# Kernel tuning notes

Hardware: AMD Instinct MI355X
Metric: run time of the kernel (lower is better)

Reference implementation:

```python
import jax, jax.numpy as jnp
import numpy as np

N = 100000          # num nodes
E = 3200000         # num edges (avg degree 32)
C = 64              # num_classes
L = 10000           # num labeled nodes
NUM_LAYERS = 10
ALPHA = 0.9


def setup_inputs() -> dict:
    key = jax.random.key(0)
    k1, k2, k3, k4 = jax.random.split(key, 4)
    y_soft = jax.random.normal(k1, (N, C), dtype=jnp.float32)
    y_true = jax.random.randint(k2, (L,), 0, C)
    mask = jax.random.randint(k3, (L,), 0, N)
    edge_index = jax.random.randint(k4, (2, E), 0, N)
    return {"y_soft": y_soft, "y_true": y_true, "mask": mask,
            "edge_index": edge_index}


def reference(y_soft, y_true, mask, edge_index):
    row, col = edge_index[0], edge_index[1]  # source -> target

    # smooth(): normalize predictions, then clamp labeled nodes to one-hot y
    z = jax.nn.softmax(y_soft, axis=1)                       # [N, C]
    y_onehot = jax.nn.one_hot(y_true, C, dtype=z.dtype)      # [L, C]
    z = z.at[mask].set(y_onehot)

    # gcn_norm without self-loops: w_e = deg^-1/2[row] * deg^-1/2[col]
    ones = jnp.ones((edge_index.shape[1],), dtype=z.dtype)
    deg = jax.ops.segment_sum(ones, col, num_segments=N)     # [N]
    dinv = jnp.where(deg > 0,
                     jax.lax.rsqrt(jnp.maximum(deg, 1e-12)),
                     jnp.zeros_like(deg))
    norm = dinv[row] * dinv[col]                             # [E]

    # Label spreading: Z <- clip(alpha * (D^-1/2 A D^-1/2) Z + (1-alpha) Z0, 0, 1)
    res = (1.0 - ALPHA) * z
    out = z
    for _ in range(NUM_LAYERS):
        msg = norm[:, None] * out[row]                       # [E, C] gather
        agg = jax.ops.segment_sum(msg, col, num_segments=N)  # [N, C] scatter-add
        out = jnp.clip(ALPHA * agg + res, 0.0, 1.0)          # PyG post_step clamp
    return out
```

## Files before the change

kernel.cpp:

```cpp
#include <hip/hip_runtime.h>
#include <hip/hip_fp16.h>

#define NCLS 64
#define ALPHA 0.9f
#define SCAN_BS 256
#define SCAN_CHUNK 1024
#define NBUCK 256
#define BSHIFT 9
#define BSPAN 512
#define P1_CAP 3200

__device__ __forceinline__ float wave_max64(float v) {
    #pragma unroll
    for (int o = 32; o > 0; o >>= 1) v = fmaxf(v, __shfl_xor(v, o, 64));
    return v;
}
__device__ __forceinline__ float wave_sum64(float v) {
    #pragma unroll
    for (int o = 32; o > 0; o >>= 1) v += __shfl_xor(v, o, 64);
    return v;
}

__global__ void winner_k(const int* __restrict__ mask, int* __restrict__ winner, int L) {
    int i = blockIdx.x * blockDim.x + threadIdx.x;
    if (i < L) atomicMax(&winner[mask[i]], i);
}

__global__ void deg_k(const int* __restrict__ col, int* __restrict__ deg, int E) {
    int stride = gridDim.x * blockDim.x;
    for (int e = blockIdx.x * blockDim.x + threadIdx.x; e < E; e += stride)
        atomicAdd(&deg[col[e]], 1);
}

__global__ void dinv_k(const int* __restrict__ deg, float* __restrict__ dinv, int n_nodes) {
    int i = blockIdx.x * blockDim.x + threadIdx.x;
    if (i < n_nodes) {
        int d = deg[i];
        dinv[i] = (d > 0) ? rsqrtf((float)d) : 0.0f;
    }
}

__global__ void scan_local_k(const int* __restrict__ deg, int* __restrict__ rowptr,
                             int* __restrict__ bsum, int n) {
    __shared__ int lds[SCAN_BS];
    int base = blockIdx.x * SCAN_CHUNK;
    int t = threadIdx.x;
    int v[4];
    int s = 0;
    #pragma unroll
    for (int k = 0; k < 4; ++k) {
        int i = base + t * 4 + k;
        v[k] = (i < n) ? deg[i] : 0;
        s += v[k];
    }
    lds[t] = s;
    __syncthreads();
    for (int o = 1; o < SCAN_BS; o <<= 1) {
        int x = (t >= o) ? lds[t - o] : 0;
        __syncthreads();
        lds[t] += x;
        __syncthreads();
    }
    int ex = (t > 0) ? lds[t - 1] : 0;
    #pragma unroll
    for (int k = 0; k < 4; ++k) {
        int i = base + t * 4 + k;
        if (i < n) rowptr[i] = ex;
        ex += v[k];
    }
    if (t == SCAN_BS - 1) bsum[blockIdx.x] = lds[t];
}

__global__ void scan_bsum_k(int* __restrict__ bsum, int nb) {
    __shared__ int lds[SCAN_BS];
    int t = threadIdx.x;
    int v = (t < nb) ? bsum[t] : 0;
    lds[t] = v;
    __syncthreads();
    for (int o = 1; o < SCAN_BS; o <<= 1) {
        int x = (t >= o) ? lds[t - o] : 0;
        __syncthreads();
        lds[t] += x;
        __syncthreads();
    }
    if (t < nb) bsum[t] = lds[t] - v;
}

__global__ void scan_add_k(int* __restrict__ rowptr, const int* __restrict__ bsum, int n) {
    int i = blockIdx.x * blockDim.x + threadIdx.x;
    if (i < n) rowptr[i] += bsum[i / SCAN_CHUNK];
}

__global__ void bcur_init_k(const int* __restrict__ rowptr, int* __restrict__ bcur,
                            int Nn, int E) {
    int b = threadIdx.x;
    int n = b * BSPAN;
    bcur[b] = (n < Nn) ? rowptr[n] : E;
}

__global__ void binpass1_k(const int* __restrict__ row, const int* __restrict__ col,
                           int* __restrict__ bcur, uint2* __restrict__ bpairs,
                           int E, int chunk) {
    __shared__ int hist[NBUCK];
    __shared__ int scn[NBUCK];
    __shared__ int lbase[NBUCK];
    __shared__ int lcur[NBUCK];
    __shared__ uint2 pairs[P1_CAP];
    int t = threadIdx.x;
    int e0 = blockIdx.x * chunk;
    int e1 = min(e0 + chunk, E);
    if (e0 >= E) return;
    hist[t] = 0;
    __syncthreads();
    for (int e = e0 + t; e < e1; e += 256)
        atomicAdd(&hist[col[e] >> BSHIFT], 1);
    __syncthreads();
    scn[t] = hist[t];
    __syncthreads();
    for (int o = 1; o < 256; o <<= 1) {
        int y = (t >= o) ? scn[t - o] : 0;
        __syncthreads();
        scn[t] += y;
        __syncthreads();
    }
    int cnt = hist[t];
    int lstart = scn[t] - cnt;
    int gb = 0;
    if (cnt > 0) gb = atomicAdd(&bcur[t], cnt);
    lbase[t] = gb - lstart;
    lcur[t] = lstart;
    __syncthreads();
    for (int e = e0 + t; e < e1; e += 256) {
        int c = col[e];
        int b = c >> BSHIFT;
        int p = atomicAdd(&lcur[b], 1);
        pairs[p] = make_uint2((unsigned)row[e], (unsigned)c);
    }
    __syncthreads();
    int n = e1 - e0;
    for (int i = t; i < n; i += 256) {
        uint2 pr = pairs[i];
        int b = (int)(pr.y >> BSHIFT);
        bpairs[lbase[b] + i] = pr;
    }
}

__global__ void binpass2_k(const int* __restrict__ rowptr, const uint2* __restrict__ bpairs,
                           int* __restrict__ src, int Nn, int E) {
    __shared__ int cur[BSPAN];
    int b = blockIdx.x;
    int nb0 = b * BSPAN;
    if (nb0 >= Nn) return;
    int nb1 = min(nb0 + BSPAN, Nn);
    int t = threadIdx.x;
    for (int i = nb0 + t; i < nb1; i += 256) cur[i - nb0] = rowptr[i];
    __syncthreads();
    int e0 = rowptr[nb0];
    int e1 = (nb1 < Nn) ? rowptr[nb1] : E;
    for (int e = e0 + t; e < e1; e += 256) {
        uint2 pr = bpairs[e];
        int p = atomicAdd(&cur[(int)pr.y - nb0], 1);
        src[p] = (int)pr.x;
    }
}

__global__ void init_k(const float* __restrict__ y, const int* __restrict__ winner,
                       const int* __restrict__ ytrue, const float* __restrict__ dinv,
                       __half* __restrict__ res_h, __half* __restrict__ vh, int Nn) {
    int lane = threadIdx.x & 63;
    int wave = (blockIdx.x * blockDim.x + threadIdx.x) >> 6;
    int nwaves = (gridDim.x * blockDim.x) >> 6;
    for (int n = wave; n < Nn; n += nwaves) {
        float v = y[(size_t)n * NCLS + lane];
        float m = wave_max64(v);
        float e = expf(v - m);
        float s = wave_sum64(e);
        float u = e / s;
        int w = winner[n];
        if (w >= 0) u = (lane == ytrue[w]) ? 1.0f : 0.0f;
        res_h[(size_t)n * NCLS + lane] = __float2half((1.0f - ALPHA) * u);
        vh[(size_t)n * NCLS + lane] = __float2half(dinv[n] * u);
    }
}

__global__ void pull_k(const int* __restrict__ rowptr, const int* __restrict__ deg,
                       const int* __restrict__ src, const float* __restrict__ dinv,
                       const __half2* __restrict__ vin2, const __half2* __restrict__ res2,
                       __half2* __restrict__ vout2, float2* __restrict__ uout2,
                       int n_nodes, int last) {
    int lane = threadIdx.x & 63;
    int half_id = lane >> 5;
    int k = lane & 31;
    int n = (blockIdx.x * blockDim.x + threadIdx.x) >> 6;
    if (n >= n_nodes) return;
    int start = rowptr[n];
    int len = deg[n];
    float2 a0 = make_float2(0.f, 0.f), a1 = make_float2(0.f, 0.f);
    float2 a2 = make_float2(0.f, 0.f), a3 = make_float2(0.f, 0.f);
    for (int base = 0; base < len; base += 64) {
        int m = min(64, len - base);
        int sv = (lane < m) ? __builtin_nontemporal_load(&src[start + base + lane]) : 0;
        int j = 0;
        for (; j + 8 <= m; j += 8) {
            int sA = __shfl(sv, j     + half_id, 64);
            int sB = __shfl(sv, j + 2 + half_id, 64);
            int sC = __shfl(sv, j + 4 + half_id, 64);
            int sD = __shfl(sv, j + 6 + half_id, 64);
            float2 fA = __half22float2(vin2[(size_t)sA * 32 + k]);
            float2 fB = __half22float2(vin2[(size_t)sB * 32 + k]);
            float2 fC = __half22float2(vin2[(size_t)sC * 32 + k]);
            float2 fD = __half22float2(vin2[(size_t)sD * 32 + k]);
            a0.x += fA.x; a0.y += fA.y;
            a1.x += fB.x; a1.y += fB.y;
            a2.x += fC.x; a2.y += fC.y;
            a3.x += fD.x; a3.y += fD.y;
        }
        for (; j + 2 <= m; j += 2) {
            int sA = __shfl(sv, j + half_id, 64);
            float2 fA = __half22float2(vin2[(size_t)sA * 32 + k]);
            a0.x += fA.x; a0.y += fA.y;
        }
        if (j < m) {
            int sA = __shfl(sv, j, 64);
            float2 fA = __half22float2(vin2[(size_t)sA * 32 + k]);
            if (half_id == 0) { a0.x += fA.x; a0.y += fA.y; }
        }
    }
    float sx = (a0.x + a1.x) + (a2.x + a3.x);
    float sy = (a0.y + a1.y) + (a2.y + a3.y);
    sx += __shfl_xor(sx, 32, 64);
    sy += __shfl_xor(sy, 32, 64);
    float di = dinv[n];
    unsigned rraw = __builtin_nontemporal_load(
        reinterpret_cast<const unsigned*>(&res2[(size_t)n * 32 + k]));
    union { unsigned u; __half2 h; } cv; cv.u = rraw;
    float2 r = __half22float2(cv.h);
    float u0 = fminf(fmaxf(ALPHA * (di * sx) + r.x, 0.0f), 1.0f);
    float u1 = fminf(fmaxf(ALPHA * (di * sy) + r.y, 0.0f), 1.0f);
    if (lane < 32) {
        size_t idx = (size_t)n * 32 + k;
        if (last) uout2[idx] = make_float2(u0, u1);
        else      vout2[idx] = __floats2half2_rn(di * u0, di * u1);
    }
}

extern "C" void kernel_launch(void* const* d_in, const int* in_sizes, int n_in,
                              void* d_out, int out_size, void* d_ws, size_t ws_size,
                              hipStream_t stream) {
    const float* y_soft = (const float*)d_in[0];
    const int* y_true  = (const int*)d_in[1];
    const int* mask    = (const int*)d_in[2];
    const int* edge    = (const int*)d_in[3];

    const int NC = in_sizes[0];
    const int Nn = NC / NCLS;
    const int L  = in_sizes[1];
    const int E  = in_sizes[3] / 2;

    const int* row = edge;
    const int* col = edge + E;

    float2* uout2 = (float2*)d_out;

    char* ws = (char*)d_ws;
    size_t off = 0;
    auto alloc = [&](size_t bytes) { char* p = ws + off; off += (bytes + 255) & ~(size_t)255; return p; };
    size_t reg0 = (size_t)E * 8;
    size_t vh_bytes = (size_t)NC * 2;
    if (2 * vh_bytes > reg0) reg0 = 2 * vh_bytes;
    char* region0 = alloc(reg0);
    uint2* bpairs = (uint2*)region0;
    __half* vhA   = (__half*)region0;
    __half* vhB   = (__half*)(region0 + vh_bytes);
    __half* res_h = (__half*)alloc((size_t)NC * 2);
    int*   src    = (int*)alloc((size_t)E * 4);
    int*   deg    = (int*)alloc((size_t)Nn * 4);
    int*   rowptr = (int*)alloc((size_t)Nn * 4);
    float* dinv   = (float*)alloc((size_t)Nn * 4);
    int*   winner = (int*)alloc((size_t)Nn * 4);
    int*   bcur   = (int*)alloc((size_t)NBUCK * 4);
    int*   bsum   = (int*)alloc((size_t)SCAN_BS * 4);

    const int NB = (Nn + SCAN_CHUNK - 1) / SCAN_CHUNK;

    hipMemsetAsync(deg, 0, (size_t)Nn * 4, stream);
    hipMemsetAsync(winner, 0xFF, (size_t)Nn * 4, stream);

    deg_k<<<2048, 256, 0, stream>>>(col, deg, E);
    dinv_k<<<(Nn + 255) / 256, 256, 0, stream>>>(deg, dinv, Nn);
    scan_local_k<<<NB, SCAN_BS, 0, stream>>>(deg, rowptr, bsum, Nn);
    scan_bsum_k<<<1, SCAN_BS, 0, stream>>>(bsum, NB);
    scan_add_k<<<(Nn + 255) / 256, 256, 0, stream>>>(rowptr, bsum, Nn);
    bcur_init_k<<<1, NBUCK, 0, stream>>>(rowptr, bcur, Nn, E);
    const int chunk = P1_CAP;
    const int nchunks = (E + chunk - 1) / chunk;
    binpass1_k<<<nchunks, 256, 0, stream>>>(row, col, bcur, bpairs, E, chunk);
    binpass2_k<<<(Nn + BSPAN - 1) / BSPAN, 256, 0, stream>>>(rowptr, bpairs, src, Nn, E);

    winner_k<<<(L + 255) / 256, 256, 0, stream>>>(mask, winner, L);
    init_k<<<2048, 256, 0, stream>>>(y_soft, winner, y_true, dinv, res_h, vhA, Nn);

    const int pull_blocks = (Nn * NCLS + 255) / 256;
    for (int it = 0; it < 10; ++it) {
        const __half2* vin2 = (const __half2*)((it & 1) ? vhB : vhA);
        __half2* vout2      = (__half2*)((it & 1) ? vhA : vhB);
        pull_k<<<pull_blocks, 256, 0, stream>>>(rowptr, deg, src, dinv,
                                                vin2, (const __half2*)res_h,
                                                vout2, uout2, Nn, it == 9);
    }
}
```

Measured before the change: 955.0 us.

## Compute degrees from bucketed edges and pack binned pairs into 32-bit words

Replaces the global per-edge atomic degree count with a coarse bucket histogram, followed by bucketing, and then a per-bucket LDS histogram that yields deg and dinv. Binned edge pairs are packed into one 32-bit word (9-bit local column offset plus 23-bit row) instead of a uint2, which halves the intermediate write and read traffic. The aim is to remove three million scattered global atomics and reduce memory traffic in the CSR build. The cost is an extra bucket-count kernel and pass, and the packing assumes fewer than 2^23 nodes.

```diff
diff --git a/kernel.cpp b/kernel.cpp
--- a/kernel.cpp
+++ b/kernel.cpp
@@ -9,6 +9,7 @@
 #define BSHIFT 9
 #define BSPAN 512
 #define P1_CAP 3200
+#define ROWMASK 0x7FFFFFu
 
 __device__ __forceinline__ float wave_max64(float v) {
     #pragma unroll
@@ -26,17 +27,112 @@
     if (i < L) atomicMax(&winner[mask[i]], i);
 }
 
-__global__ void deg_k(const int* __restrict__ col, int* __restrict__ deg, int E) {
+__global__ void bcount_k(const int* __restrict__ col, int* __restrict__ bcnt, int E) {
+    __shared__ int h[NBUCK];
+    int t = threadIdx.x;
+    h[t] = 0;
+    __syncthreads();
     int stride = gridDim.x * blockDim.x;
-    for (int e = blockIdx.x * blockDim.x + threadIdx.x; e < E; e += stride)
-        atomicAdd(&deg[col[e]], 1);
-}
-
-__global__ void dinv_k(const int* __restrict__ deg, float* __restrict__ dinv, int n_nodes) {
-    int i = blockIdx.x * blockDim.x + threadIdx.x;
-    if (i < n_nodes) {
-        int d = deg[i];
-        dinv[i] = (d > 0) ? rsqrtf((float)d) : 0.0f;
+    for (int e = blockIdx.x * blockDim.x + t; e < E; e += stride)
+        atomicAdd(&h[col[e] >> BSHIFT], 1);
+    __syncthreads();
+    if (h[t]) atomicAdd(&bcnt[t], h[t]);
+}
+
+__global__ void bscan_k(const int* __restrict__ bcnt, int* __restrict__ bbase,
+                        int* __restrict__ bcur, int E) {
+    __shared__ int lds[NBUCK];
+    int t = threadIdx.x;
+    int v = bcnt[t];
+    lds[t] = v;
+    __syncthreads();
+    for (int o = 1; o < NBUCK; o <<= 1) {
+        int x = (t >= o) ? lds[t - o] : 0;
+        __syncthreads();
+        lds[t] += x;
+        __syncthreads();
+    }
+    int ex = lds[t] - v;
+    bbase[t] = ex;
+    bcur[t] = ex;
+    if (t == NBUCK - 1) bbase[NBUCK] = E;
+}
+
+__global__ void binpass1_k(const int* __restrict__ row, const int* __restrict__ col,
+                           int* __restrict__ bcur, unsigned* __restrict__ bpk,
+                           int E, int chunk) {
+    __shared__ int hist[NBUCK];
+    __shared__ int scn[NBUCK];
+    __shared__ int lbase[NBUCK];
+    __shared__ int lcur[NBUCK];
+    __shared__ unsigned pay[P1_CAP];
+    __shared__ unsigned char bkt[P1_CAP];
+    int t = threadIdx.x;
+    int e0 = blockIdx.x * chunk;
+    int e1 = min(e0 + chunk, E);
+    if (e0 >= E) return;
+    hist[t] = 0;
+    __syncthreads();
+    for (int e = e0 + t; e < e1; e += 256)
+        atomicAdd(&hist[col[e] >> BSHIFT], 1);
+    __syncthreads();
+    scn[t] = hist[t];
+    __syncthreads();
+    for (int o = 1; o < 256; o <<= 1) {
+        int y = (t >= o) ? scn[t - o] : 0;
+        __syncthreads();
+        scn[t] += y;
+        __syncthreads();
+    }
+    int cnt = hist[t];
+    int lstart = scn[t] - cnt;
+    int gb = 0;
+    if (cnt > 0) gb = atomicAdd(&bcur[t], cnt);
+    lbase[t] = gb - lstart;
+    lcur[t] = lstart;
+    __syncthreads();
+    for (int e = e0 + t; e < e1; e += 256) {
+        int c = col[e];
+        int b = c >> BSHIFT;
+        int p = atomicAdd(&lcur[b], 1);
+        pay[p] = ((unsigned)(c & (BSPAN - 1)) << 23) | (unsigned)row[e];
+        bkt[p] = (unsigned char)b;
+    }
+    __syncthreads();
+    int n = e1 - e0;
+    for (int i = t; i < n; i += 256) {
+        unsigned w = pay[i];
+        int b = bkt[i];
+        bpk[lbase[b] + i] = w;
+    }
+}
+
+__global__ void bdeg_k(const int* __restrict__ bbase, const unsigned* __restrict__ bpk,
+                       int* __restrict__ deg, float* __restrict__ dinv, int Nn) {
+    __shared__ int hist[BSPAN];
+    int b = blockIdx.x;
+    int nb0 = b * BSPAN;
+    if (nb0 >= Nn) return;
+    int t = threadIdx.x;
+    hist[t] = 0;
+    hist[t + 256] = 0;
+    __syncthreads();
+    int e0 = bbase[b];
+    int e1 = bbase[b + 1];
+    for (int e = e0 + t; e < e1; e += 256)
+        atomicAdd(&hist[bpk[e] >> 23], 1);
+    __syncthreads();
+    int n0 = nb0 + t;
+    if (n0 < Nn) {
+        int d = hist[t];
+        deg[n0] = d;
+        dinv[n0] = (d > 0) ? rsqrtf((float)d) : 0.0f;
+    }
+    int n1 = nb0 + 256 + t;
+    if (n1 < Nn) {
+        int d = hist[t + 256];
+        deg[n1] = d;
+        dinv[n1] = (d > 0) ? rsqrtf((float)d) : 0.0f;
     }
 }
 
@@ -91,61 +187,7 @@
     if (i < n) rowptr[i] += bsum[i / SCAN_CHUNK];
 }
 
-__global__ void bcur_init_k(const int* __restrict__ rowptr, int* __restrict__ bcur,
-                            int Nn, int E) {
-    int b = threadIdx.x;
-    int n = b * BSPAN;
-    bcur[b] = (n < Nn) ? rowptr[n] : E;
-}
-
-__global__ void binpass1_k(const int* __restrict__ row, const int* __restrict__ col,
-                           int* __restrict__ bcur, uint2* __restrict__ bpairs,
-                           int E, int chunk) {
-    __shared__ int hist[NBUCK];
-    __shared__ int scn[NBUCK];
-    __shared__ int lbase[NBUCK];
-    __shared__ int lcur[NBUCK];
-    __shared__ uint2 pairs[P1_CAP];
-    int t = threadIdx.x;
-    int e0 = blockIdx.x * chunk;
-    int e1 = min(e0 + chunk, E);
-    if (e0 >= E) return;
-    hist[t] = 0;
-    __syncthreads();
-    for (int e = e0 + t; e < e1; e += 256)
-        atomicAdd(&hist[col[e] >> BSHIFT], 1);
-    __syncthreads();
-    scn[t] = hist[t];
-    __syncthreads();
-    for (int o = 1; o < 256; o <<= 1) {
-        int y = (t >= o) ? scn[t - o] : 0;
-        __syncthreads();
-        scn[t] += y;
-        __syncthreads();
-    }
-    int cnt = hist[t];
-    int lstart = scn[t] - cnt;
-    int gb = 0;
-    if (cnt > 0) gb = atomicAdd(&bcur[t], cnt);
-    lbase[t] = gb - lstart;
-    lcur[t] = lstart;
-    __syncthreads();
-    for (int e = e0 + t; e < e1; e += 256) {
-        int c = col[e];
-        int b = c >> BSHIFT;
-        int p = atomicAdd(&lcur[b], 1);
-        pairs[p] = make_uint2((unsigned)row[e], (unsigned)c);
-    }
-    __syncthreads();
-    int n = e1 - e0;
-    for (int i = t; i < n; i += 256) {
-        uint2 pr = pairs[i];
-        int b = (int)(pr.y >> BSHIFT);
-        bpairs[lbase[b] + i] = pr;
-    }
-}
-
-__global__ void binpass2_k(const int* __restrict__ rowptr, const uint2* __restrict__ bpairs,
+__global__ void binpass2_k(const int* __restrict__ rowptr, const unsigned* __restrict__ bpk,
                            int* __restrict__ src, int Nn, int E) {
     __shared__ int cur[BSPAN];
     int b = blockIdx.x;
@@ -158,9 +200,9 @@
     int e0 = rowptr[nb0];
     int e1 = (nb1 < Nn) ? rowptr[nb1] : E;
     for (int e = e0 + t; e < e1; e += 256) {
-        uint2 pr = bpairs[e];
-        int p = atomicAdd(&cur[(int)pr.y - nb0], 1);
-        src[p] = (int)pr.x;
+        unsigned w = bpk[e];
+        int p = atomicAdd(&cur[w >> 23], 1);
+        src[p] = (int)(w & ROWMASK);
     }
 }
 
@@ -265,11 +307,11 @@
     char* ws = (char*)d_ws;
     size_t off = 0;
     auto alloc = [&](size_t bytes) { char* p = ws + off; off += (bytes + 255) & ~(size_t)255; return p; };
-    size_t reg0 = (size_t)E * 8;
+    size_t reg0 = (size_t)E * 4;
     size_t vh_bytes = (size_t)NC * 2;
     if (2 * vh_bytes > reg0) reg0 = 2 * vh_bytes;
     char* region0 = alloc(reg0);
-    uint2* bpairs = (uint2*)region0;
+    unsigned* bpk = (unsigned*)region0;
     __half* vhA   = (__half*)region0;
     __half* vhB   = (__half*)(region0 + vh_bytes);
     __half* res_h = (__half*)alloc((size_t)NC * 2);
@@ -278,26 +320,30 @@
     int*   rowptr = (int*)alloc((size_t)Nn * 4);
     float* dinv   = (float*)alloc((size_t)Nn * 4);
     int*   winner = (int*)alloc((size_t)Nn * 4);
+    int*   bcnt   = (int*)alloc((size_t)NBUCK * 4);
+    int*   bbase  = (int*)alloc((size_t)(NBUCK + 1) * 4);
     int*   bcur   = (int*)alloc((size_t)NBUCK * 4);
     int*   bsum   = (int*)alloc((size_t)SCAN_BS * 4);
 
     const int NB = (Nn + SCAN_CHUNK - 1) / SCAN_CHUNK;
-
-    hipMemsetAsync(deg, 0, (size_t)Nn * 4, stream);
+    const int NBK = (Nn + BSPAN - 1) / BSPAN;
+
     hipMemsetAsync(winner, 0xFF, (size_t)Nn * 4, stream);
-
-    deg_k<<<2048, 256, 0, stream>>>(col, deg, E);
-    dinv_k<<<(Nn + 255) / 256, 256, 0, stream>>>(deg, dinv, Nn);
+    hipMemsetAsync(bcnt, 0, (size_t)NBUCK * 4, stream);
+
+    winner_k<<<(L + 255) / 256, 256, 0, stream>>>(mask, winner, L);
+
+    bcount_k<<<1024, 256, 0, stream>>>(col, bcnt, E);
+    bscan_k<<<1, NBUCK, 0, stream>>>(bcnt, bbase, bcur, E);
+    const int chunk = P1_CAP;
+    const int nchunks = (E + chunk - 1) / chunk;
+    binpass1_k<<<nchunks, 256, 0, stream>>>(row, col, bcur, bpk, E, chunk);
+    bdeg_k<<<NBK, 256, 0, stream>>>(bbase, bpk, deg, dinv, Nn);
     scan_local_k<<<NB, SCAN_BS, 0, stream>>>(deg, rowptr, bsum, Nn);
     scan_bsum_k<<<1, SCAN_BS, 0, stream>>>(bsum, NB);
     scan_add_k<<<(Nn + 255) / 256, 256, 0, stream>>>(rowptr, bsum, Nn);
-    bcur_init_k<<<1, NBUCK, 0, stream>>>(rowptr, bcur, Nn, E);
-    const int chunk = P1_CAP;
-    const int nchunks = (E + chunk - 1) / chunk;
-    binpass1_k<<<nchunks, 256, 0, stream>>>(row, col, bcur, bpairs, E, chunk);
-    binpass2_k<<<(Nn + BSPAN - 1) / BSPAN, 256, 0, stream>>>(rowptr, bpairs, src, Nn, E);
-
-    winner_k<<<(L + 255) / 256, 256, 0, stream>>>(mask, winner, L);
+    binpass2_k<<<NBK, 256, 0, stream>>>(rowptr, bpk, src, Nn, E);
+
     init_k<<<2048, 256, 0, stream>>>(y_soft, winner, y_true, dinv, res_h, vhA, Nn);
 
     const int pull_blocks = (Nn * NCLS + 255) / 256;
```

Measured after the change: 863.7 us. -9.6%, faster.
